# Optimization experiments

Hardware: AMD Instinct MI355X
Metric: run time of the kernel (lower is better)

## Reference

```python
import jax, jax.numpy as jnp
import numpy as np

T, B, D, H, R, O = 32, 8, 512, 512, 32, 512
CLIP_VAL = 1.0
LN_EPS = 1e-5


def setup_inputs() -> dict:
    key = jax.random.key(0)
    ks = jax.random.split(key, 8)
    rn = lambda k, sh, sc: (jax.random.normal(k, sh) * sc).astype(jnp.float32)
    inp = {
        'x': rn(ks[0], (T, B, D), 1.0),
        'h0': jnp.zeros((B, H), jnp.float32),
        'v0': jnp.zeros((B, H), jnp.float32),
        'dU0': jnp.zeros((B, H, H), jnp.float32),
        'trace_e0': jnp.zeros((B, H), jnp.float32),
        'trace_E0': jnp.zeros((B, H, H), jnp.float32),
        # parameters (init-scale approximations of the torch inits)
        'x2h_w': rn(ks[1], (2 * H, D), 1.0 / np.sqrt(D)),
        'x2h_b': jnp.zeros((2 * H,), jnp.float32),
        'h2h_w': rn(ks[2], (2 * H, H), 1.0 / np.sqrt(H)),
        'h2h_b': jnp.zeros((2 * H,), jnp.float32),
        'lnx_g': jnp.ones((2 * H,), jnp.float32),
        'lnx_b': jnp.zeros((2 * H,), jnp.float32),
        'lnh_g': jnp.ones((2 * H,), jnp.float32),
        'lnh_b': jnp.zeros((2 * H,), jnp.float32),
        'h2mod_w': rn(ks[3], (R, H), np.sqrt(2.0 / H)),
        'h2mod_b': jnp.zeros((R,), jnp.float32),
        'mod2h_w': rn(ks[4], (3, R), np.sqrt(2.0 / R)),
        'mod2h_b': jnp.zeros((3,), jnp.float32),
        'alpha': jnp.full((1,), -4.0, jnp.float32),
        'tau_U': jnp.full((1,), -4.5, jnp.float32),
        'dec_w': rn(ks[5], (O, H), 1.0 / np.sqrt(H)),
        'dec_b': jnp.zeros((O,), jnp.float32),
    }
    return inp


def _ln(y, g, b):
    mu = jnp.mean(y, axis=-1, keepdims=True)
    yc = y - mu
    var = jnp.mean(yc * yc, axis=-1, keepdims=True)
    return g * yc * jax.lax.rsqrt(var + LN_EPS) + b


def reference(x, h0, v0, dU0, trace_e0, trace_E0,
              x2h_w, x2h_b, h2h_w, h2h_b,
              lnx_g, lnx_b, lnh_g, lnh_b,
              h2mod_w, h2mod_b, mod2h_w, mod2h_b,
              alpha, tau_U, dec_w, dec_b):
    Hh = h0.shape[-1]
    sp_alpha = jax.nn.softplus(alpha)            # (1,)
    tau = jax.nn.sigmoid(tau_U)                  # (1,)
    # clip bounds derived from the candidate-row block of h2h weight
    w_dv = h2h_w[Hh:2 * Hh]                      # [H, H]
    upper = jax.nn.relu(CLIP_VAL - w_dv) / (sp_alpha + 1e-8)
    lower = -jax.nn.relu(CLIP_VAL + w_dv) / (sp_alpha + 1e-8)

    def step(carry, xt):
        h, v, dU, te, tE = carry
        Wx = _ln(xt @ x2h_w.T + x2h_b, lnx_g, lnx_b)           # [B, 2H]
        Wh = h @ h2h_w.T + h2h_b                               # [B, 2H]
        plast = sp_alpha * jnp.einsum('bij,bj->bi', dU, h)     # [B, H]
        Wh = Wh.at[:, Hh:].add(plast)
        Wh = _ln(Wh, lnh_g, lnh_b)
        z, dv = jnp.split(Wx + Wh, 2, axis=-1)
        z = jax.nn.sigmoid(z)
        v_n = (1.0 - z) * v + z * dv
        nh = jax.nn.relu(v_n)
        mod = jax.nn.relu(nh @ h2mod_w.T + h2mod_b) @ mod2h_w.T + mod2h_b  # [B, 3]
        r = jax.nn.sigmoid(mod[:, :1])                          # [B, 1]
        s = jax.nn.sigmoid(mod[:, 1])[:, None, None]            # [B, 1, 1]
        m = mod[:, 2][:, None, None]                            # [B, 1, 1]
        te_n = (1.0 - r) * te + r * h
        outer = nh[:, :, None] * te_n[:, None, :]               # [B, H, H]
        tE_n = (1.0 - s) * tE + s * (outer - jnp.swapaxes(outer, 1, 2))
        dU_n = (1.0 - tau) * dU + tau * m * tE_n
        dU_n = jnp.where(dU_n > upper, upper, dU_n)
        dU_n = jnp.where(dU_n < lower, lower, dU_n)
        return (nh, v_n, dU_n, te_n, tE_n), nh

    carry0 = (h0, v0, dU0, trace_e0, trace_E0)
    _, hs = jax.lax.scan(step, carry0, x)                        # hs: [T, B, H]
    out = hs @ dec_w.T + dec_b                                   # [T, B, O]
    return out
```

## Files before the change

kernel.cpp:

```cpp
#include <hip/hip_runtime.h>

#define TT 32
#define BB 8
#define DD 512
#define HH 512
#define RR 32
#define OO 512
#define H2 1024

#define OFF_WX    0
#define OFF_HS    262144
#define OFF_COLV  393216
#define OFF_FLAGS 409600

#define AGENT __HIP_MEMORY_SCOPE_AGENT
#define RLX   __ATOMIC_RELAXED

__device__ __forceinline__ void st_coh(float* p, float v) {
  __hip_atomic_store(p, v, RLX, AGENT);
}
__device__ __forceinline__ float ld_coh(const float* p) {
  return __hip_atomic_load(const_cast<float*>(p), RLX, AGENT);
}
__device__ __forceinline__ float d4(const float4& a, const float4& b) {
  return a.x*b.x + a.y*b.y + a.z*b.z + a.w*b.w;
}

__device__ __forceinline__ void bar32(unsigned* flags, int b, int ir,
                                      unsigned seq, int tid) {
  __syncthreads();
  asm volatile("s_waitcnt vmcnt(0)" ::: "memory");
  if (tid == 0)
    __hip_atomic_store(&flags[b*32 + ir], seq, RLX, AGENT);
  if (tid < 64) {
    for (;;) {
      unsigned v = (tid < 32) ? __hip_atomic_load(&flags[b*32 + tid], RLX, AGENT) : seq;
      if (__all(v >= seq)) break;
      __builtin_amdgcn_s_sleep(1);
    }
  }
  __syncthreads();
}

template<bool UPDATE>
__device__ __forceinline__ void gemv_step(
    int gi, int m,
    float4 (&dUr)[4], float4 (&tEr)[4],
    const float4 (&Wdvr)[4], const float4 (&wlo)[4],
    const float4 (&upr)[4], const float4 (&lor)[4],
    float s_b, float c1t, float c2t, float a_sp, float hbl, float hbh,
    const float* nh_s, const float* te_s,
    float* post)
{
  const float nh_i = nh_s[gi];
  const float te_i = UPDATE ? te_s[gi] : 0.0f;
  const float4* nh4 = reinterpret_cast<const float4*>(nh_s);
  const float4* te4 = reinterpret_cast<const float4*>(te_s);
  float plast = 0.0f, gdv = 0.0f, glo = 0.0f;
#pragma unroll
  for (int q = 0; q < 4; ++q) {
    const int J = m + 32*q;
    const float4 h4 = nh4[J];
    if (UPDATE) {
      const float4 t4 = te4[J];
#define SGRU_UPD(C) { \
      float o   = nh_i * t4.C - h4.C * te_i;                 \
      float tEn = tEr[q].C + s_b * (o - tEr[q].C);           \
      tEr[q].C  = tEn;                                                               \
      float d   = c1t * dUr[q].C + c2t * tEn;                \
      d = fminf(d, upr[q].C); d = fmaxf(d, lor[q].C);        \
      dUr[q].C  = d;                                                                 \
      plast = fmaf(d, h4.C, plast); }
      SGRU_UPD(x) SGRU_UPD(y) SGRU_UPD(z) SGRU_UPD(w)
#undef SGRU_UPD
    } else {
      plast += d4(dUr[q], h4);
    }
    gdv += d4(Wdvr[q], h4);
    glo += d4(wlo[q],  h4);
  }
#pragma unroll
  for (int off = 16; off >= 1; off >>= 1) {
    plast += __shfl_xor(plast, off);
    gdv   += __shfl_xor(gdv, off);
    glo   += __shfl_xor(glo, off);
  }
  if (m == 0) {
    st_coh(&post[gi],      glo + hbl);
    st_coh(&post[HH + gi], gdv + hbh + a_sp * plast);
  }
}

__global__ __launch_bounds__(512, 1) void sgru_persistent(
    const float* __restrict__ h0,     const float* __restrict__ v0,
    const float* __restrict__ dU0,    const float* __restrict__ tE0,
    const float* __restrict__ te0,
    const float* __restrict__ h2h_w,  const float* __restrict__ h2h_b,
    const float* __restrict__ lnh_g,  const float* __restrict__ lnh_b,
    const float* __restrict__ h2mod_w,const float* __restrict__ h2mod_b,
    const float* __restrict__ mod2h_w,const float* __restrict__ mod2h_b,
    const float* __restrict__ alpha_p,const float* __restrict__ tau_p,
    float* __restrict__ ws)
{
  const int tid = threadIdx.x;
  const int b   = blockIdx.x & 7;
  const int ir  = blockIdx.x >> 3;
  const int i0  = ir << 4;
  const int il  = tid >> 5;
  const int m   = tid & 31;
  const int gi  = i0 + il;

  const float* Wx = ws + OFF_WX;
  float* hsbuf    = ws + OFF_HS;
  float* colvG    = ws + OFF_COLV;
  unsigned* flags = (unsigned*)(ws + OFF_FLAGS);

  __shared__ float nh_s[2][HH];
  __shared__ float te_s[HH];
  __shared__ float hmw_s[RR * 516];
  __shared__ float mp_s[RR];
  __shared__ float rsm_s[4];
  __shared__ float red_s[2][8];

  const float a_sp  = log1pf(__expf(alpha_p[0]));
  const float inv_a = 1.0f / (a_sp + 1e-8f);
  const float tau   = 1.0f / (1.0f + __expf(-tau_p[0]));
  const float c1t   = 1.0f - tau;

  float4 dUr[4], tEr[4], Wdvr[4], wlo[4], upr[4], lor[4];
  {
    const size_t rowoff = ((size_t)b * HH + gi) * HH;
    const size_t whioff = (size_t)(HH + gi) * HH;
    const size_t wlooff = (size_t)gi * HH;
#pragma unroll
    for (int q = 0; q < 4; ++q) {
      const int J = m + 32*q;
      dUr[q] = *reinterpret_cast<const float4*>(dU0 + rowoff + 4*J);
      tEr[q] = *reinterpret_cast<const float4*>(tE0 + rowoff + 4*J);
      wlo[q] = *reinterpret_cast<const float4*>(h2h_w + wlooff + 4*J);
      const float4 w = *reinterpret_cast<const float4*>(h2h_w + whioff + 4*J);
      Wdvr[q] = w;
      float4 u, l;
      u.x =  fmaxf(1.0f - w.x, 0.0f) * inv_a;  l.x = -fmaxf(1.0f + w.x, 0.0f) * inv_a;
      u.y =  fmaxf(1.0f - w.y, 0.0f) * inv_a;  l.y = -fmaxf(1.0f + w.y, 0.0f) * inv_a;
      u.z =  fmaxf(1.0f - w.z, 0.0f) * inv_a;  l.z = -fmaxf(1.0f + w.z, 0.0f) * inv_a;
      u.w =  fmaxf(1.0f - w.w, 0.0f) * inv_a;  l.w = -fmaxf(1.0f + w.w, 0.0f) * inv_a;
      upr[q] = u; lor[q] = l;
    }
  }

  const float rgz = lnh_g[tid],      rbz = lnh_b[tid];
  const float rgd = lnh_g[HH + tid], rbd = lnh_b[HH + tid];
  const float hbl = h2h_b[gi], hbh = h2h_b[HH + gi];
  const float hmb = h2mod_b[tid >> 4];
  const float mw0 = (tid < RR) ? mod2h_w[tid]        : 0.0f;
  const float mw1 = (tid < RR) ? mod2h_w[RR + tid]   : 0.0f;
  const float mw2 = (tid < RR) ? mod2h_w[2*RR + tid] : 0.0f;
  const float mb0 = mod2h_b[0], mb1 = mod2h_b[1], mb2 = mod2h_b[2];
  float vreg = v0[b*HH + tid];

  nh_s[1][tid] = h0[b*HH + tid];
  te_s[tid]    = te0[b*HH + tid];
  for (int idx = tid; idx < RR*HH; idx += 512)
    hmw_s[(idx >> 9)*516 + (idx & 511)] = h2mod_w[idx];
  __syncthreads();

  gemv_step<false>(gi, m, dUr, tEr, Wdvr, wlo, upr, lor,
                   0.0f, c1t, 0.0f, a_sp, hbl, hbh,
                   nh_s[1], te_s, colvG + 0*BB*H2 + b*H2);

  float wxz = Wx[(size_t)(0*BB + b)*H2 + tid];
  float wxd = Wx[(size_t)(0*BB + b)*H2 + HH + tid];

  unsigned seq = 0;
  for (int t = 0; t < TT; ++t) {
    const int cur = t & 1;
    bar32(flags, b, ir, ++seq, tid);

    const float whz = ld_coh(&colvG[cur*BB*H2 + b*H2 + tid]);
    const float whd = ld_coh(&colvG[cur*BB*H2 + b*H2 + HH + tid]);

    float s1 = whz + whd, s2 = whz*whz + whd*whd;
#pragma unroll
    for (int off = 32; off >= 1; off >>= 1) {
      s1 += __shfl_xor(s1, off);
      s2 += __shfl_xor(s2, off);
    }
    if ((tid & 63) == 0) { red_s[0][tid >> 6] = s1; red_s[1][tid >> 6] = s2; }
    __syncthreads();
    s1 = 0.0f; s2 = 0.0f;
#pragma unroll
    for (int w = 0; w < 8; ++w) { s1 += red_s[0][w]; s2 += red_s[1][w]; }
    const float mu   = s1 * (1.0f / H2);
    const float var  = s2 * (1.0f / H2) - mu * mu;
    const float rstd = rsqrtf(var + 1e-5f);

    const float yz = (whz - mu)*rstd*rgz + rbz + wxz;
    const float yd = (whd - mu)*rstd*rgd + rbd + wxd;
    const float z  = 1.0f / (1.0f + __expf(-yz));
    vreg = vreg + z * (yd - vreg);
    const float nh = fmaxf(vreg, 0.0f);
    nh_s[cur][tid] = nh;
    if (ir == 0) hsbuf[(size_t)(t*BB + b)*HH + tid] = nh;
    if (t == TT - 1) return;

    wxz = Wx[(size_t)((t+1)*BB + b)*H2 + tid];
    wxd = Wx[(size_t)((t+1)*BB + b)*H2 + HH + tid];
    __syncthreads();

    {
      const int r = tid >> 4, kk = tid & 15;
      float part = 0.0f;
#pragma unroll
      for (int j = 0; j < 32; ++j)
        part += hmw_s[r*516 + kk + 16*j] * nh_s[cur][kk + 16*j];
#pragma unroll
      for (int off = 8; off >= 1; off >>= 1) part += __shfl_xor(part, off);
      if (kk == 0) mp_s[r] = fmaxf(part + hmb, 0.0f);
    }
    __syncthreads();
    if (tid < 64) {
      const float mp = (tid < RR) ? mp_s[tid] : 0.0f;
      float a0 = mw0*mp, a1 = mw1*mp, a2 = mw2*mp;
#pragma unroll
      for (int off = 16; off >= 1; off >>= 1) {
        a0 += __shfl_xor(a0, off);
        a1 += __shfl_xor(a1, off);
        a2 += __shfl_xor(a2, off);
      }
      if (tid == 0) {
        rsm_s[0] = 1.0f / (1.0f + __expf(-(a0 + mb0)));
        rsm_s[1] = 1.0f / (1.0f + __expf(-(a1 + mb1)));
        rsm_s[2] = a2 + mb2;
      }
    }
    __syncthreads();
    const float r_b = rsm_s[0];
    const float s_b = rsm_s[1];
    const float c2t = tau * rsm_s[2];

    te_s[tid] += r_b * (nh_s[1 - cur][tid] - te_s[tid]);
    __syncthreads();

    gemv_step<true>(gi, m, dUr, tEr, Wdvr, wlo, upr, lor,
                    s_b, c1t, c2t, a_sp, hbl, hbh,
                    nh_s[cur], te_s, colvG + (1 - cur)*BB*H2 + b*H2);
  }
}

#define GBM 64
#define GBN 32
#define GBK 32
__global__ __launch_bounds__(256) void gemm_tn(
    const float* __restrict__ A, const float* __restrict__ W,
    const float* __restrict__ bias, float* __restrict__ C,
    int M, int N)
{
  const int K = 512;
  const int nbn = N / GBN;
  const int m0 = (blockIdx.x / nbn) * GBM;
  const int n0 = (blockIdx.x % nbn) * GBN;
  const int tid = threadIdx.x;
  const int tx = tid & 15;
  const int ty = tid >> 4;
  const int lr = tid >> 3;
  const int lc = tid & 7;
  __shared__ float As[GBK][68];
  __shared__ float Ws[GBK][36];
  float acc[4][2] = {};
  for (int kc = 0; kc < K; kc += GBK) {
    const float4 a0 = *reinterpret_cast<const float4*>(A + (size_t)(m0 + lr)*K      + kc + lc*4);
    const float4 a1 = *reinterpret_cast<const float4*>(A + (size_t)(m0 + lr + 32)*K + kc + lc*4);
    const float4 w0 = *reinterpret_cast<const float4*>(W + (size_t)(n0 + lr)*K      + kc + lc*4);
    __syncthreads();
    As[lc*4+0][lr] = a0.x; As[lc*4+1][lr] = a0.y; As[lc*4+2][lr] = a0.z; As[lc*4+3][lr] = a0.w;
    As[lc*4+0][lr+32] = a1.x; As[lc*4+1][lr+32] = a1.y; As[lc*4+2][lr+32] = a1.z; As[lc*4+3][lr+32] = a1.w;
    Ws[lc*4+0][lr] = w0.x; Ws[lc*4+1][lr] = w0.y; Ws[lc*4+2][lr] = w0.z; Ws[lc*4+3][lr] = w0.w;
    __syncthreads();
#pragma unroll
    for (int k = 0; k < GBK; ++k) {
      const float4 am = *reinterpret_cast<const float4*>(&As[k][ty*4]);
      const float2 wn = *reinterpret_cast<const float2*>(&Ws[k][tx*2]);
      acc[0][0] += am.x*wn.x; acc[0][1] += am.x*wn.y;
      acc[1][0] += am.y*wn.x; acc[1][1] += am.y*wn.y;
      acc[2][0] += am.z*wn.x; acc[2][1] += am.z*wn.y;
      acc[3][0] += am.w*wn.x; acc[3][1] += am.w*wn.y;
    }
  }
  const float bv0 = bias[n0 + tx*2], bv1 = bias[n0 + tx*2 + 1];
#pragma unroll
  for (int i = 0; i < 4; ++i) {
    C[(size_t)(m0 + ty*4 + i)*N + n0 + tx*2]     = acc[i][0] + bv0;
    C[(size_t)(m0 + ty*4 + i)*N + n0 + tx*2 + 1] = acc[i][1] + bv1;
  }
}

__global__ __launch_bounds__(256) void ln_apply(
    float* __restrict__ Wp, const float* __restrict__ g, const float* __restrict__ b)
{
  const int row = blockIdx.x;
  const int tid = threadIdx.x;
  float* rp = Wp + (size_t)row * H2;
  float4 v = *reinterpret_cast<const float4*>(rp + tid*4);
  float s1 = v.x + v.y + v.z + v.w;
  float s2 = v.x*v.x + v.y*v.y + v.z*v.z + v.w*v.w;
#pragma unroll
  for (int off = 32; off >= 1; off >>= 1) {
    s1 += __shfl_xor(s1, off);
    s2 += __shfl_xor(s2, off);
  }
  __shared__ float red[2][4];
  if ((tid & 63) == 0) { red[0][tid >> 6] = s1; red[1][tid >> 6] = s2; }
  __syncthreads();
  s1 = red[0][0] + red[0][1] + red[0][2] + red[0][3];
  s2 = red[1][0] + red[1][1] + red[1][2] + red[1][3];
  const float mu   = s1 * (1.0f / H2);
  const float var  = s2 * (1.0f / H2) - mu * mu;
  const float rstd = rsqrtf(var + 1e-5f);
  const float4 gv = *reinterpret_cast<const float4*>(g + tid*4);
  const float4 bv = *reinterpret_cast<const float4*>(b + tid*4);
  v.x = gv.x*(v.x - mu)*rstd + bv.x;
  v.y = gv.y*(v.y - mu)*rstd + bv.y;
  v.z = gv.z*(v.z - mu)*rstd + bv.z;
  v.w = gv.w*(v.w - mu)*rstd + bv.w;
  *reinterpret_cast<float4*>(rp + tid*4) = v;
}

extern "C" void kernel_launch(void* const* d_in, const int* in_sizes, int n_in,
                              void* d_out, int out_size, void* d_ws, size_t ws_size,
                              hipStream_t stream) {
  (void)in_sizes; (void)n_in; (void)out_size; (void)ws_size;
  const float* x        = (const float*)d_in[0];
  const float* h0       = (const float*)d_in[1];
  const float* v0       = (const float*)d_in[2];
  const float* dU0      = (const float*)d_in[3];
  const float* te0      = (const float*)d_in[4];
  const float* tE0      = (const float*)d_in[5];
  const float* x2h_w    = (const float*)d_in[6];
  const float* x2h_b    = (const float*)d_in[7];
  const float* h2h_w    = (const float*)d_in[8];
  const float* h2h_b    = (const float*)d_in[9];
  const float* lnx_g    = (const float*)d_in[10];
  const float* lnx_b    = (const float*)d_in[11];
  const float* lnh_g    = (const float*)d_in[12];
  const float* lnh_b    = (const float*)d_in[13];
  const float* h2mod_w  = (const float*)d_in[14];
  const float* h2mod_b  = (const float*)d_in[15];
  const float* mod2h_w  = (const float*)d_in[16];
  const float* mod2h_b  = (const float*)d_in[17];
  const float* alpha    = (const float*)d_in[18];
  const float* tau_U    = (const float*)d_in[19];
  const float* dec_w    = (const float*)d_in[20];
  const float* dec_b    = (const float*)d_in[21];

  float* ws = (float*)d_ws;
  unsigned* flags = (unsigned*)(ws + OFF_FLAGS);

  hipMemsetAsync(flags, 0, 256 * sizeof(unsigned), stream);

  gemm_tn<<<(TT*BB/GBM) * (H2/GBN), 256, 0, stream>>>(x, x2h_w, x2h_b,
                                                      ws + OFF_WX, TT*BB, H2);
  ln_apply<<<TT*BB, 256, 0, stream>>>(ws + OFF_WX, lnx_g, lnx_b);

  sgru_persistent<<<256, 512, 0, stream>>>(h0, v0, dU0, tE0, te0,
                                           h2h_w, h2h_b, lnh_g, lnh_b,
                                           h2mod_w, h2mod_b, mod2h_w, mod2h_b,
                                           alpha, tau_U, ws);

  gemm_tn<<<(TT*BB/GBM) * (OO/GBN), 256, 0, stream>>>(ws + OFF_HS, dec_w, dec_b,
                                                      (float*)d_out, TT*BB, OO);
}
```

Before: 194.3 us.

## Replace flag barrier with tagged 64-bit value slots and restructure step syncs

Drops the per-batch flag barrier. Each hidden-state partial is now published as a 64-bit word that packs the step tag with the float value, so consumers spin directly on the data they need. Inside a step, the recurrent GEMV half that needs no trace is computed early, the modulation reduction is replicated in every wave instead of passing through shared memory, and the trace update is double-buffered, which removes two __syncthreads per step. Slot zeroing moves into ln_apply in place of a memset. The cost is polling of per-element loads and doubled colv storage traffic.

Result: slower. 254.3 us (+30.9%).

```diff
diff --git a/kernel.cpp b/kernel.cpp
--- a/kernel.cpp
+++ b/kernel.cpp
@@ -8,88 +8,26 @@
 #define OO 512
 #define H2 1024
 
+typedef unsigned long long ull;
+
 #define OFF_WX    0
 #define OFF_HS    262144
 #define OFF_COLV  393216
-#define OFF_FLAGS 409600
 
 #define AGENT __HIP_MEMORY_SCOPE_AGENT
 #define RLX   __ATOMIC_RELAXED
 
-__device__ __forceinline__ void st_coh(float* p, float v) {
+__device__ __forceinline__ ull ld8(const ull* p) {
+  return __hip_atomic_load(const_cast<ull*>(p), RLX, AGENT);
+}
+__device__ __forceinline__ void st8(ull* p, ull v) {
   __hip_atomic_store(p, v, RLX, AGENT);
-}
-__device__ __forceinline__ float ld_coh(const float* p) {
-  return __hip_atomic_load(const_cast<float*>(p), RLX, AGENT);
 }
 __device__ __forceinline__ float d4(const float4& a, const float4& b) {
   return a.x*b.x + a.y*b.y + a.z*b.z + a.w*b.w;
 }
 
-__device__ __forceinline__ void bar32(unsigned* flags, int b, int ir,
-                                      unsigned seq, int tid) {
-  __syncthreads();
-  asm volatile("s_waitcnt vmcnt(0)" ::: "memory");
-  if (tid == 0)
-    __hip_atomic_store(&flags[b*32 + ir], seq, RLX, AGENT);
-  if (tid < 64) {
-    for (;;) {
-      unsigned v = (tid < 32) ? __hip_atomic_load(&flags[b*32 + tid], RLX, AGENT) : seq;
-      if (__all(v >= seq)) break;
-      __builtin_amdgcn_s_sleep(1);
-    }
-  }
-  __syncthreads();
-}
-
-template<bool UPDATE>
-__device__ __forceinline__ void gemv_step(
-    int gi, int m,
-    float4 (&dUr)[4], float4 (&tEr)[4],
-    const float4 (&Wdvr)[4], const float4 (&wlo)[4],
-    const float4 (&upr)[4], const float4 (&lor)[4],
-    float s_b, float c1t, float c2t, float a_sp, float hbl, float hbh,
-    const float* nh_s, const float* te_s,
-    float* post)
-{
-  const float nh_i = nh_s[gi];
-  const float te_i = UPDATE ? te_s[gi] : 0.0f;
-  const float4* nh4 = reinterpret_cast<const float4*>(nh_s);
-  const float4* te4 = reinterpret_cast<const float4*>(te_s);
-  float plast = 0.0f, gdv = 0.0f, glo = 0.0f;
-#pragma unroll
-  for (int q = 0; q < 4; ++q) {
-    const int J = m + 32*q;
-    const float4 h4 = nh4[J];
-    if (UPDATE) {
-      const float4 t4 = te4[J];
-#define SGRU_UPD(C) { \
-      float o   = nh_i * t4.C - h4.C * te_i;                 \
-      float tEn = tEr[q].C + s_b * (o - tEr[q].C);           \
-      tEr[q].C  = tEn;                                                               \
-      float d   = c1t * dUr[q].C + c2t * tEn;                \
-      d = fminf(d, upr[q].C); d = fmaxf(d, lor[q].C);        \
-      dUr[q].C  = d;                                                                 \
-      plast = fmaf(d, h4.C, plast); }
-      SGRU_UPD(x) SGRU_UPD(y) SGRU_UPD(z) SGRU_UPD(w)
-#undef SGRU_UPD
-    } else {
-      plast += d4(dUr[q], h4);
-    }
-    gdv += d4(Wdvr[q], h4);
-    glo += d4(wlo[q],  h4);
-  }
-#pragma unroll
-  for (int off = 16; off >= 1; off >>= 1) {
-    plast += __shfl_xor(plast, off);
-    gdv   += __shfl_xor(gdv, off);
-    glo   += __shfl_xor(glo, off);
-  }
-  if (m == 0) {
-    st_coh(&post[gi],      glo + hbl);
-    st_coh(&post[HH + gi], gdv + hbh + a_sp * plast);
-  }
-}
+#define HMW_P 528
 
 __global__ __launch_bounds__(512, 1) void sgru_persistent(
     const float* __restrict__ h0,     const float* __restrict__ v0,
@@ -112,14 +50,12 @@
 
   const float* Wx = ws + OFF_WX;
   float* hsbuf    = ws + OFF_HS;
-  float* colvG    = ws + OFF_COLV;
-  unsigned* flags = (unsigned*)(ws + OFF_FLAGS);
+  ull* colvT      = (ull*)(ws + OFF_COLV);
 
   __shared__ float nh_s[2][HH];
-  __shared__ float te_s[HH];
-  __shared__ float hmw_s[RR * 516];
+  __shared__ float te_s[2][HH];
+  __shared__ float hmw_s[RR * HMW_P];
   __shared__ float mp_s[RR];
-  __shared__ float rsm_s[4];
   __shared__ float red_s[2][8];
 
   const float a_sp  = log1pf(__expf(alpha_p[0]));
@@ -153,32 +89,55 @@
   const float rgd = lnh_g[HH + tid], rbd = lnh_b[HH + tid];
   const float hbl = h2h_b[gi], hbh = h2h_b[HH + gi];
   const float hmb = h2mod_b[tid >> 4];
-  const float mw0 = (tid < RR) ? mod2h_w[tid]        : 0.0f;
-  const float mw1 = (tid < RR) ? mod2h_w[RR + tid]   : 0.0f;
-  const float mw2 = (tid < RR) ? mod2h_w[2*RR + tid] : 0.0f;
+  const float mw0 = mod2h_w[tid & 31];
+  const float mw1 = mod2h_w[RR + (tid & 31)];
+  const float mw2 = mod2h_w[2*RR + (tid & 31)];
   const float mb0 = mod2h_b[0], mb1 = mod2h_b[1], mb2 = mod2h_b[2];
   float vreg = v0[b*HH + tid];
 
   nh_s[1][tid] = h0[b*HH + tid];
-  te_s[tid]    = te0[b*HH + tid];
+  te_s[0][tid] = te0[b*HH + tid];
   for (int idx = tid; idx < RR*HH; idx += 512)
-    hmw_s[(idx >> 9)*516 + (idx & 511)] = h2mod_w[idx];
+    hmw_s[(idx >> 9)*HMW_P + (idx & 511)] = h2mod_w[idx];
   __syncthreads();
 
-  gemv_step<false>(gi, m, dUr, tEr, Wdvr, wlo, upr, lor,
-                   0.0f, c1t, 0.0f, a_sp, hbl, hbh,
-                   nh_s[1], te_s, colvG + 0*BB*H2 + b*H2);
+  {
+    const float4* h4p = reinterpret_cast<const float4*>(nh_s[1]);
+    float glo = 0.0f, gdv = 0.0f, plast = 0.0f;
+#pragma unroll
+    for (int q = 0; q < 4; ++q) {
+      const float4 h4 = h4p[m + 32*q];
+      glo   += d4(wlo[q],  h4);
+      gdv   += d4(Wdvr[q], h4);
+      plast += d4(dUr[q],  h4);
+    }
+#pragma unroll
+    for (int off = 16; off >= 1; off >>= 1) {
+      glo   += __shfl_xor(glo, off);
+      gdv   += __shfl_xor(gdv, off);
+      plast += __shfl_xor(plast, off);
+    }
+    if (m == 0) {
+      ull* ps = colvT + ((size_t)(0*BB + b)*512 + gi)*2;
+      const ull tg = 1ull << 32;
+      st8(ps,     tg | (ull)__float_as_uint(glo + hbl));
+      st8(ps + 1, tg | (ull)__float_as_uint(gdv + hbh + a_sp*plast));
+    }
+  }
 
   float wxz = Wx[(size_t)(0*BB + b)*H2 + tid];
   float wxd = Wx[(size_t)(0*BB + b)*H2 + HH + tid];
 
-  unsigned seq = 0;
   for (int t = 0; t < TT; ++t) {
     const int cur = t & 1;
-    bar32(flags, b, ir, ++seq, tid);
-
-    const float whz = ld_coh(&colvG[cur*BB*H2 + b*H2 + tid]);
-    const float whd = ld_coh(&colvG[cur*BB*H2 + b*H2 + HH + tid]);
+
+    const ull* slot = colvT + (size_t)(cur*BB + b)*1024;
+    ull vz, vd;
+    const ull want = (ull)(t + 1);
+    for (;;) { vz = ld8(slot + tid*2);     if ((vz >> 32) == want) break; __builtin_amdgcn_s_sleep(1); }
+    for (;;) { vd = ld8(slot + tid*2 + 1); if ((vd >> 32) == want) break; __builtin_amdgcn_s_sleep(1); }
+    const float whz = __uint_as_float((unsigned)vz);
+    const float whd = __uint_as_float((unsigned)vd);
 
     float s1 = whz + whd, s2 = whz*whz + whd*whd;
 #pragma unroll
@@ -208,19 +167,37 @@
     wxd = Wx[(size_t)((t+1)*BB + b)*H2 + HH + tid];
     __syncthreads();
 
+    float glo = 0.0f, gdv = 0.0f;
+    float4 h4q[4];
+    {
+      const float4* nh4 = reinterpret_cast<const float4*>(nh_s[cur]);
+#pragma unroll
+      for (int q = 0; q < 4; ++q) {
+        h4q[q] = nh4[m + 32*q];
+        glo += d4(wlo[q],  h4q[q]);
+        gdv += d4(Wdvr[q], h4q[q]);
+      }
+#pragma unroll
+      for (int off = 16; off >= 1; off >>= 1) {
+        glo += __shfl_xor(glo, off);
+        gdv += __shfl_xor(gdv, off);
+      }
+    }
     {
       const int r = tid >> 4, kk = tid & 15;
       float part = 0.0f;
 #pragma unroll
       for (int j = 0; j < 32; ++j)
-        part += hmw_s[r*516 + kk + 16*j] * nh_s[cur][kk + 16*j];
+        part += hmw_s[r*HMW_P + kk + 16*j] * nh_s[cur][kk + 16*j];
 #pragma unroll
       for (int off = 8; off >= 1; off >>= 1) part += __shfl_xor(part, off);
       if (kk == 0) mp_s[r] = fmaxf(part + hmb, 0.0f);
     }
     __syncthreads();
-    if (tid < 64) {
-      const float mp = (tid < RR) ? mp_s[tid] : 0.0f;
+
+    float r_b, s_b, c2t;
+    {
+      const float mp = mp_s[tid & 31];
       float a0 = mw0*mp, a1 = mw1*mp, a2 = mw2*mp;
 #pragma unroll
       for (int off = 16; off >= 1; off >>= 1) {
@@ -228,23 +205,52 @@
         a1 += __shfl_xor(a1, off);
         a2 += __shfl_xor(a2, off);
       }
-      if (tid == 0) {
-        rsm_s[0] = 1.0f / (1.0f + __expf(-(a0 + mb0)));
-        rsm_s[1] = 1.0f / (1.0f + __expf(-(a1 + mb1)));
-        rsm_s[2] = a2 + mb2;
+      r_b = 1.0f / (1.0f + __expf(-(a0 + mb0)));
+      s_b = 1.0f / (1.0f + __expf(-(a1 + mb1)));
+      c2t = tau * (a2 + mb2);
+    }
+
+    {
+      const float teo = te_s[cur][tid];
+      te_s[1 - cur][tid] = teo + r_b * (nh_s[1 - cur][tid] - teo);
+    }
+
+    const float nh_i  = nh_s[cur][gi];
+    const float teo_i = te_s[cur][gi];
+    const float hp_i  = nh_s[1 - cur][gi];
+    const float te_i  = teo_i + r_b * (hp_i - teo_i);
+    float plast = 0.0f;
+    {
+      const float4* te4o = reinterpret_cast<const float4*>(te_s[cur]);
+      const float4* hp4  = reinterpret_cast<const float4*>(nh_s[1 - cur]);
+#pragma unroll
+      for (int q = 0; q < 4; ++q) {
+        const int J = m + 32*q;
+        const float4 h4 = h4q[q];
+        const float4 to = te4o[J];
+        const float4 hp = hp4[J];
+#define SGRU_UPD(C) { \
+        float ten = to.C + r_b * (hp.C - to.C);              \
+        float o   = nh_i * ten - h4.C * te_i;                \
+        float tEn = tEr[q].C + s_b * (o - tEr[q].C);         \
+        tEr[q].C  = tEn;                                                             \
+        float d   = c1t * dUr[q].C + c2t * tEn;              \
+        d = fminf(d, upr[q].C); d = fmaxf(d, lor[q].C);      \
+        dUr[q].C  = d;                                                               \
+        plast = fmaf(d, h4.C, plast); }
+        SGRU_UPD(x) SGRU_UPD(y) SGRU_UPD(z) SGRU_UPD(w)
+#undef SGRU_UPD
       }
-    }
-    __syncthreads();
-    const float r_b = rsm_s[0];
-    const float s_b = rsm_s[1];
-    const float c2t = tau * rsm_s[2];
-
-    te_s[tid] += r_b * (nh_s[1 - cur][tid] - te_s[tid]);
-    __syncthreads();
-
-    gemv_step<true>(gi, m, dUr, tEr, Wdvr, wlo, upr, lor,
-                    s_b, c1t, c2t, a_sp, hbl, hbh,
-                    nh_s[cur], te_s, colvG + (1 - cur)*BB*H2 + b*H2);
+#pragma unroll
+      for (int off = 16; off >= 1; off >>= 1) plast += __shfl_xor(plast, off);
+    }
+
+    if (m == 0) {
+      ull* ps = colvT + ((size_t)((1 - cur)*BB + b)*512 + gi)*2;
+      const ull tg = (ull)(t + 2) << 32;
+      st8(ps,     tg | (ull)__float_as_uint(glo + hbl));
+      st8(ps + 1, tg | (ull)__float_as_uint(gdv + hbh + a_sp*plast));
+    }
   }
 }
 
@@ -296,10 +302,15 @@
 }
 
 __global__ __launch_bounds__(256) void ln_apply(
-    float* __restrict__ Wp, const float* __restrict__ g, const float* __restrict__ b)
+    float* __restrict__ Wp, const float* __restrict__ g, const float* __restrict__ b,
+    ull* __restrict__ colvT)
 {
   const int row = blockIdx.x;
   const int tid = threadIdx.x;
+  {
+    const int idx = row * 256 + tid;
+    if (idx < 2*BB*512*2) colvT[idx] = 0ull;
+  }
   float* rp = Wp + (size_t)row * H2;
   float4 v = *reinterpret_cast<const float4*>(rp + tid*4);
   float s1 = v.x + v.y + v.z + v.w;
@@ -354,13 +365,11 @@
   const float* dec_b    = (const float*)d_in[21];
 
   float* ws = (float*)d_ws;
-  unsigned* flags = (unsigned*)(ws + OFF_FLAGS);
-
-  hipMemsetAsync(flags, 0, 256 * sizeof(unsigned), stream);
 
   gemm_tn<<<(TT*BB/GBM) * (H2/GBN), 256, 0, stream>>>(x, x2h_w, x2h_b,
                                                       ws + OFF_WX, TT*BB, H2);
-  ln_apply<<<TT*BB, 256, 0, stream>>>(ws + OFF_WX, lnx_g, lnx_b);
+  ln_apply<<<TT*BB, 256, 0, stream>>>(ws + OFF_WX, lnx_g, lnx_b,
+                                      (ull*)(ws + OFF_COLV));
 
   sgru_persistent<<<256, 512, 0, stream>>>(h0, v0, dU0, tE0, te0,
                                            h2h_w, h2h_b, lnh_g, lnh_b,
```

## Fold flag reset into ln_apply, shrink GEMM M-tile, repad h2mod smem

Applied to the files above, without the earlier changes.

Removes the separate hipMemsetAsync on the barrier flags and instead zeroes them inside the ln_apply kernel, cutting one stream operation. Halves the GEMM M tile from 64 to 32, doubling the block count for better occupancy on the small projection GEMMs at the cost of less reuse per block. Changes the row padding of the h2mod weight in shared memory from 516 to 528 floats, which changes the LDS bank mapping of its reads.

Result: faster. 174.7 us (-10.1%).

```diff
diff --git a/kernel.cpp b/kernel.cpp
--- a/kernel.cpp
+++ b/kernel.cpp
@@ -8,6 +8,8 @@
 #define OO 512
 #define H2 1024
 
+typedef unsigned int uint;
+
 #define OFF_WX    0
 #define OFF_HS    262144
 #define OFF_COLV  393216
@@ -15,6 +17,8 @@
 
 #define AGENT __HIP_MEMORY_SCOPE_AGENT
 #define RLX   __ATOMIC_RELAXED
+
+#define HMW_P 528
 
 __device__ __forceinline__ void st_coh(float* p, float v) {
   __hip_atomic_store(p, v, RLX, AGENT);
@@ -117,7 +121,7 @@
 
   __shared__ float nh_s[2][HH];
   __shared__ float te_s[HH];
-  __shared__ float hmw_s[RR * 516];
+  __shared__ float hmw_s[RR * HMW_P];
   __shared__ float mp_s[RR];
   __shared__ float rsm_s[4];
   __shared__ float red_s[2][8];
@@ -162,7 +166,7 @@
   nh_s[1][tid] = h0[b*HH + tid];
   te_s[tid]    = te0[b*HH + tid];
   for (int idx = tid; idx < RR*HH; idx += 512)
-    hmw_s[(idx >> 9)*516 + (idx & 511)] = h2mod_w[idx];
+    hmw_s[(idx >> 9)*HMW_P + (idx & 511)] = h2mod_w[idx];
   __syncthreads();
 
   gemv_step<false>(gi, m, dUr, tEr, Wdvr, wlo, upr, lor,
@@ -213,7 +217,7 @@
       float part = 0.0f;
 #pragma unroll
       for (int j = 0; j < 32; ++j)
-        part += hmw_s[r*516 + kk + 16*j] * nh_s[cur][kk + 16*j];
+        part += hmw_s[r*HMW_P + kk + 16*j] * nh_s[cur][kk + 16*j];
 #pragma unroll
       for (int off = 8; off >= 1; off >>= 1) part += __shfl_xor(part, off);
       if (kk == 0) mp_s[r] = fmaxf(part + hmb, 0.0f);
@@ -248,7 +252,7 @@
   }
 }
 
-#define GBM 64
+#define GBM 32
 #define GBN 32
 #define GBK 32
 __global__ __launch_bounds__(256) void gemm_tn(
@@ -265,41 +269,38 @@
   const int ty = tid >> 4;
   const int lr = tid >> 3;
   const int lc = tid & 7;
-  __shared__ float As[GBK][68];
+  __shared__ float As[GBK][36];
   __shared__ float Ws[GBK][36];
-  float acc[4][2] = {};
+  float acc[2][2] = {};
   for (int kc = 0; kc < K; kc += GBK) {
-    const float4 a0 = *reinterpret_cast<const float4*>(A + (size_t)(m0 + lr)*K      + kc + lc*4);
-    const float4 a1 = *reinterpret_cast<const float4*>(A + (size_t)(m0 + lr + 32)*K + kc + lc*4);
-    const float4 w0 = *reinterpret_cast<const float4*>(W + (size_t)(n0 + lr)*K      + kc + lc*4);
+    const float4 a0 = *reinterpret_cast<const float4*>(A + (size_t)(m0 + lr)*K + kc + lc*4);
+    const float4 w0 = *reinterpret_cast<const float4*>(W + (size_t)(n0 + lr)*K + kc + lc*4);
     __syncthreads();
     As[lc*4+0][lr] = a0.x; As[lc*4+1][lr] = a0.y; As[lc*4+2][lr] = a0.z; As[lc*4+3][lr] = a0.w;
-    As[lc*4+0][lr+32] = a1.x; As[lc*4+1][lr+32] = a1.y; As[lc*4+2][lr+32] = a1.z; As[lc*4+3][lr+32] = a1.w;
     Ws[lc*4+0][lr] = w0.x; Ws[lc*4+1][lr] = w0.y; Ws[lc*4+2][lr] = w0.z; Ws[lc*4+3][lr] = w0.w;
     __syncthreads();
 #pragma unroll
     for (int k = 0; k < GBK; ++k) {
-      const float4 am = *reinterpret_cast<const float4*>(&As[k][ty*4]);
+      const float2 am = *reinterpret_cast<const float2*>(&As[k][ty*2]);
       const float2 wn = *reinterpret_cast<const float2*>(&Ws[k][tx*2]);
       acc[0][0] += am.x*wn.x; acc[0][1] += am.x*wn.y;
       acc[1][0] += am.y*wn.x; acc[1][1] += am.y*wn.y;
-      acc[2][0] += am.z*wn.x; acc[2][1] += am.z*wn.y;
-      acc[3][0] += am.w*wn.x; acc[3][1] += am.w*wn.y;
-    }
-  }
-  const float bv0 = bias[n0 + tx*2], bv1 = bias[n0 + tx*2 + 1];
-#pragma unroll
-  for (int i = 0; i < 4; ++i) {
-    C[(size_t)(m0 + ty*4 + i)*N + n0 + tx*2]     = acc[i][0] + bv0;
-    C[(size_t)(m0 + ty*4 + i)*N + n0 + tx*2 + 1] = acc[i][1] + bv1;
-  }
+    }
+  }
+  const float b0 = bias[n0 + tx*2], b1 = bias[n0 + tx*2 + 1];
+  C[(size_t)(m0 + ty*2 + 0)*N + n0 + tx*2]     = acc[0][0] + b0;
+  C[(size_t)(m0 + ty*2 + 0)*N + n0 + tx*2 + 1] = acc[0][1] + b1;
+  C[(size_t)(m0 + ty*2 + 1)*N + n0 + tx*2]     = acc[1][0] + b0;
+  C[(size_t)(m0 + ty*2 + 1)*N + n0 + tx*2 + 1] = acc[1][1] + b1;
 }
 
 __global__ __launch_bounds__(256) void ln_apply(
-    float* __restrict__ Wp, const float* __restrict__ g, const float* __restrict__ b)
+    float* __restrict__ Wp, const float* __restrict__ g, const float* __restrict__ b,
+    unsigned* __restrict__ flags)
 {
   const int row = blockIdx.x;
   const int tid = threadIdx.x;
+  if (row == 0) flags[tid] = 0u;
   float* rp = Wp + (size_t)row * H2;
   float4 v = *reinterpret_cast<const float4*>(rp + tid*4);
   float s1 = v.x + v.y + v.z + v.w;
@@ -354,13 +355,11 @@
   const float* dec_b    = (const float*)d_in[21];
 
   float* ws = (float*)d_ws;
-  unsigned* flags = (unsigned*)(ws + OFF_FLAGS);
-
-  hipMemsetAsync(flags, 0, 256 * sizeof(unsigned), stream);
 
   gemm_tn<<<(TT*BB/GBM) * (H2/GBN), 256, 0, stream>>>(x, x2h_w, x2h_b,
                                                       ws + OFF_WX, TT*BB, H2);
-  ln_apply<<<TT*BB, 256, 0, stream>>>(ws + OFF_WX, lnx_g, lnx_b);
+  ln_apply<<<TT*BB, 256, 0, stream>>>(ws + OFF_WX, lnx_g, lnx_b,
+                                      (unsigned*)(ws + OFF_FLAGS));
 
   sgru_persistent<<<256, 512, 0, stream>>>(h0, v0, dU0, tE0, te0,
                                            h2h_w, h2h_b, lnh_g, lnh_b,
```
